# Kernel optimization log

Hardware: AMD Instinct MI355X
Metric: run time of the kernel (lower is better)

The kernel has to match this reference:

```python
import jax, jax.numpy as jnp
import numpy as np


def setup_inputs() -> dict:
    key = jax.random.key(0)
    k1, k2 = jax.random.split(key)
    N = 2_000_000
    rotation = jax.random.normal(k1, (N, 3, 3), dtype=jnp.float32)
    # learned parameter: eye(3) + 0.001 * randn(3,3)
    mat = jnp.eye(3, dtype=jnp.float32) + 0.001 * jax.random.normal(k2, (3, 3), dtype=jnp.float32)
    return {"rotation": rotation, "mat": mat}


def reference(rotation, mat):
    # new_mat[n] = rotation[n] @ mat   (mat broadcast over the batch)
    new_mat = jnp.einsum('nab,bc->nac', rotation, mat)
    # batched 3x3 SVD; polar orthogonal factor U @ V^T
    U, S, Vh = jnp.linalg.svd(new_mat, full_matrices=False)
    out = jnp.einsum('nab,nbc->nac', U, Vh)  # Vh is already V^T
    logdet = jnp.zeros((rotation.shape[0],), dtype=rotation.dtype)
    return out, logdet
```

## Files before the change

### kernel.cpp

```cpp
#include <hip/hip_runtime.h>
#include <math.h>

constexpr int BLOCK = 256;
constexpr int WPB = 4;

typedef __attribute__((address_space(3))) uint32_t lds_u32_t;
typedef __attribute__((address_space(1))) const uint32_t glb_u32_t;

__device__ __forceinline__ void issue_tile_loads(
    const float* __restrict__ rot, long long tile, int lane, float* buf)
{
    const char* g = (const char*)rot + (size_t)tile * 2304;
    __builtin_amdgcn_global_load_lds((glb_u32_t*)(g + (size_t)lane * 16),
                                     (lds_u32_t*)buf, 16, 0, 0);
    __builtin_amdgcn_global_load_lds((glb_u32_t*)(g + 1024 + (size_t)lane * 16),
                                     (lds_u32_t*)(buf + 256), 16, 0, 0);
    __builtin_amdgcn_global_load_lds((glb_u32_t*)(g + 2048 + (size_t)lane * 4),
                                     (lds_u32_t*)(buf + 512), 4, 0, 0);
}

__device__ __forceinline__ void polar_core_h(
    const float r0, const float r1, const float r2,
    const float r3, const float r4, const float r5,
    const float r6, const float r7, const float r8,
    const float m0, const float m1, const float m2,
    const float m3, const float m4, const float m5,
    const float m6, const float m7, const float m8,
    float& x0, float& x1, float& x2,
    float& x3, float& x4, float& x5,
    float& x6, float& x7, float& x8)
{
    const double dR = (double)r0*((double)r4*r8-(double)r5*r7)
                    - (double)r1*((double)r3*r8-(double)r5*r6)
                    + (double)r2*((double)r3*r7-(double)r4*r6);
    const float detA = (float)dR;

    x0=fmaf(r0,m0,fmaf(r1,m3,r2*m6));
    x1=fmaf(r0,m1,fmaf(r1,m4,r2*m7));
    x2=fmaf(r0,m2,fmaf(r1,m5,r2*m8));
    x3=fmaf(r3,m0,fmaf(r4,m3,r5*m6));
    x4=fmaf(r3,m1,fmaf(r4,m4,r5*m7));
    x5=fmaf(r3,m2,fmaf(r4,m5,r5*m8));
    x6=fmaf(r6,m0,fmaf(r7,m3,r8*m6));
    x7=fmaf(r6,m1,fmaf(r7,m4,r8*m7));
    x8=fmaf(r6,m2,fmaf(r7,m5,r8*m8));

    {
        const float c0=fmaf(x4,x8,-x5*x7), c1=fmaf(x5,x6,-x3*x8), c2=fmaf(x3,x7,-x4*x6);
        const float c3=fmaf(x2,x7,-x1*x8), c4=fmaf(x0,x8,-x2*x6), c5=fmaf(x1,x6,-x0*x7);
        const float c6=fmaf(x1,x5,-x2*x4), c7=fmaf(x2,x3,-x0*x5), c8=fmaf(x0,x4,-x1*x3);
        const float adet = fmaxf(fabsf(detA), 1e-30f);
        float nX2, nC2;
        { const float a=fmaf(x1,x1,x0*x0), b=fmaf(x3,x3,x2*x2),
                      e=fmaf(x5,x5,x4*x4), d=fmaf(x7,x7,x6*x6);
          nX2=(a+b)+(e+fmaf(x8,x8,d)); }
        { const float a=fmaf(c1,c1,c0*c0), b=fmaf(c3,c3,c2*c2),
                      e=fmaf(c5,c5,c4*c4), d=fmaf(c7,c7,c6*c6);
          nC2=(a+b)+(e+fmaf(c8,c8,d)); }
        const float h  = __builtin_amdgcn_rsqf(adet);
        const float pr = __builtin_amdgcn_sqrtf(__builtin_amdgcn_sqrtf(
                             nC2*__builtin_amdgcn_rcpf(nX2)));
        const float qr = __builtin_amdgcn_rcpf(pr);
        const float s = 0.5f*pr*h;
        const float t = copysignf(0.5f*qr*h, detA);
        x0=fmaf(s,x0,t*c0); x1=fmaf(s,x1,t*c1); x2=fmaf(s,x2,t*c2);
        x3=fmaf(s,x3,t*c3); x4=fmaf(s,x4,t*c4); x5=fmaf(s,x5,t*c5);
        x6=fmaf(s,x6,t*c6); x7=fmaf(s,x7,t*c7); x8=fmaf(s,x8,t*c8);
    }
    #pragma unroll
    for (int it = 0; it < 4; ++it) {
        const float c0=fmaf(x4,x8,-x5*x7), c1=fmaf(x5,x6,-x3*x8), c2=fmaf(x3,x7,-x4*x6);
        const float c3=fmaf(x2,x7,-x1*x8), c4=fmaf(x0,x8,-x2*x6), c5=fmaf(x1,x6,-x0*x7);
        const float c6=fmaf(x1,x5,-x2*x4), c7=fmaf(x2,x3,-x0*x5), c8=fmaf(x0,x4,-x1*x3);
        const float det = fmaf(x0,c0,fmaf(x1,c1,x2*c2));
        const float adet = fmaxf(fabsf(det), 1e-30f);
        const float mu = __builtin_amdgcn_exp2f(
                             -0.33333333f*__builtin_amdgcn_logf(adet));
        const float s = 0.5f*mu;
        const float t = copysignf(0.5f*__builtin_amdgcn_rcpf(mu*adet), det);
        x0=fmaf(s,x0,t*c0); x1=fmaf(s,x1,t*c1); x2=fmaf(s,x2,t*c2);
        x3=fmaf(s,x3,t*c3); x4=fmaf(s,x4,t*c4); x5=fmaf(s,x5,t*c5);
        x6=fmaf(s,x6,t*c6); x7=fmaf(s,x7,t*c7); x8=fmaf(s,x8,t*c8);
    }
    {
        const float c0=fmaf(x4,x8,-x5*x7), c1=fmaf(x5,x6,-x3*x8), c2=fmaf(x3,x7,-x4*x6);
        const float c3=fmaf(x2,x7,-x1*x8), c4=fmaf(x0,x8,-x2*x6), c5=fmaf(x1,x6,-x0*x7);
        const float c6=fmaf(x1,x5,-x2*x4), c7=fmaf(x2,x3,-x0*x5), c8=fmaf(x0,x4,-x1*x3);
        const float det = fmaf(x0,c0,fmaf(x1,c1,x2*c2));
        const float t = 0.5f*__builtin_amdgcn_rcpf(det);
        x0=fmaf(0.5f,x0,t*c0); x1=fmaf(0.5f,x1,t*c1); x2=fmaf(0.5f,x2,t*c2);
        x3=fmaf(0.5f,x3,t*c3); x4=fmaf(0.5f,x4,t*c4); x5=fmaf(0.5f,x5,t*c5);
        x6=fmaf(0.5f,x6,t*c6); x7=fmaf(0.5f,x7,t*c7); x8=fmaf(0.5f,x8,t*c8);
    }
}

__global__ __launch_bounds__(BLOCK) void polar3x3_kernel(
    const float* __restrict__ rot,
    const float* __restrict__ mat,
    float* __restrict__ outq,
    float* __restrict__ logdet,
    int N)
{
    __shared__ float lds[WPB * 2 * 576];
    const int lane = threadIdx.x & 63;
    const int wave = threadIdx.x >> 6;
    const long long W   = (long long)gridDim.x * WPB;
    const long long wid = (long long)blockIdx.x * WPB + wave;
    const int NT = N >> 6;

    const float m0=mat[0], m1=mat[1], m2=mat[2], m3=mat[3], m4=mat[4],
                m5=mat[5], m6=mat[6], m7=mat[7], m8=mat[8];
    asm volatile("s_waitcnt vmcnt(0) lgkmcnt(0)" ::: "memory");

    long long t = wid;
    if (t < NT) {
        float* bc = lds + wave * 1152;
        float* bn = bc + 576;
        issue_tile_loads(rot, t, lane, bc);
        { const long long t1 = t + W;
          issue_tile_loads(rot, (t1 < NT) ? t1 : 0, lane, bn); }
        asm volatile("s_waitcnt vmcnt(3)" ::: "memory");

        for (; t < NT; t += W) {
            const float* r = &bc[lane * 9];
            const float r0=r[0],r1=r[1],r2=r[2],r3=r[3],r4=r[4],
                        r5=r[5],r6=r[6],r7=r[7],r8=r[8];
            float x0,x1,x2,x3,x4,x5,x6,x7,x8;
            polar_core_h(r0,r1,r2,r3,r4,r5,r6,r7,r8,
                         m0,m1,m2,m3,m4,m5,m6,m7,m8,
                         x0,x1,x2,x3,x4,x5,x6,x7,x8);

            float* w = &bc[lane * 9];
            w[0]=x0; w[1]=x1; w[2]=x2; w[3]=x3; w[4]=x4;
            w[5]=x5; w[6]=x6; w[7]=x7; w[8]=x8;
            asm volatile("s_waitcnt lgkmcnt(0)" ::: "memory");

            const long long mb = t * 64;
            float* gdst = outq + mb * 9;
            const float4* l4 = (const float4*)bc;
            float4* g4 = (float4*)gdst;
            g4[lane]         = l4[lane];
            g4[64 + lane]    = l4[64 + lane];
            gdst[512 + lane] = bc[512 + lane];
            logdet[mb + lane] = 0.0f;

            asm volatile("" ::: "memory");

            { const long long tn = t + 2*W;
              issue_tile_loads(rot, (tn < NT) ? tn : 0, lane, bc); }

            asm volatile("s_waitcnt vmcnt(7)" ::: "memory");

            float* tmp = bc; bc = bn; bn = tmp;
        }
    }

    const int rem = N - NT * 64;
    if (rem > 0 && wid == 0) {
        const long long tb = (long long)NT * 64;
        const bool act = lane < rem;
        float r0=1.f,r1=0.f,r2=0.f,r3=0.f,r4=1.f,r5=0.f,r6=0.f,r7=0.f,r8=1.f;
        const float* gsrc = rot + (tb + lane) * 9;
        if (act) { r0=gsrc[0];r1=gsrc[1];r2=gsrc[2];r3=gsrc[3];r4=gsrc[4];
                   r5=gsrc[5];r6=gsrc[6];r7=gsrc[7];r8=gsrc[8]; }
        float x0,x1,x2,x3,x4,x5,x6,x7,x8;
        polar_core_h(r0,r1,r2,r3,r4,r5,r6,r7,r8,
                     m0,m1,m2,m3,m4,m5,m6,m7,m8,
                     x0,x1,x2,x3,x4,x5,x6,x7,x8);
        if (act) {
            float* gdst = outq + (tb + lane) * 9;
            gdst[0]=x0; gdst[1]=x1; gdst[2]=x2; gdst[3]=x3; gdst[4]=x4;
            gdst[5]=x5; gdst[6]=x6; gdst[7]=x7; gdst[8]=x8;
            logdet[tb + lane] = 0.0f;
        }
    }
}

extern "C" void kernel_launch(void* const* d_in, const int* in_sizes, int n_in,
                              void* d_out, int out_size, void* d_ws, size_t ws_size,
                              hipStream_t stream) {
    const float* rot = (const float*)d_in[0];
    const float* mat = (const float*)d_in[1];
    float* out = (float*)d_out;
    const int N = in_sizes[0] / 9;
    float* logdet = out + (long long)N * 9;
    const int NT = N >> 6;
    long long nb = ((long long)NT + WPB - 1) / WPB;
    if (nb > 2048) nb = 2048;
    if (nb < 1) nb = 1;
    polar3x3_kernel<<<(int)nb, BLOCK, 0, stream>>>(rot, mat, out, logdet, N);
}
```

Before: 139.4 us.

## Warp-specialize block into a loader wave and three compute waves

```diff
diff --git a/kernel.cpp b/kernel.cpp
--- a/kernel.cpp
+++ b/kernel.cpp
@@ -2,10 +2,16 @@
 #include <math.h>
 
 constexpr int BLOCK = 256;
-constexpr int WPB = 4;
+constexpr int NCONS = 3;
+constexpr int NSLOT = 3;
 
 typedef __attribute__((address_space(3))) uint32_t lds_u32_t;
 typedef __attribute__((address_space(1))) const uint32_t glb_u32_t;
+
+#define FENCE() asm volatile("" ::: "memory")
+__device__ __forceinline__ void BAR() {
+    FENCE(); __builtin_amdgcn_s_barrier(); FENCE();
+}
 
 __device__ __forceinline__ void issue_tile_loads(
     const float* __restrict__ rot, long long tile, int lane, float* buf)
@@ -101,62 +107,72 @@
     float* __restrict__ logdet,
     int N)
 {
-    __shared__ float lds[WPB * 2 * 576];
+    __shared__ float lds[NCONS * NSLOT * 576];
     const int lane = threadIdx.x & 63;
     const int wave = threadIdx.x >> 6;
-    const long long W   = (long long)gridDim.x * WPB;
-    const long long wid = (long long)blockIdx.x * WPB + wave;
     const int NT = N >> 6;
+    const long long CW = (long long)gridDim.x * NCONS;
+    const int nrounds = (int)(((long long)NT + CW - 1) / CW);
 
     const float m0=mat[0], m1=mat[1], m2=mat[2], m3=mat[3], m4=mat[4],
                 m5=mat[5], m6=mat[6], m7=mat[7], m8=mat[8];
     asm volatile("s_waitcnt vmcnt(0) lgkmcnt(0)" ::: "memory");
 
-    long long t = wid;
-    if (t < NT) {
-        float* bc = lds + wave * 1152;
-        float* bn = bc + 576;
-        issue_tile_loads(rot, t, lane, bc);
-        { const long long t1 = t + W;
-          issue_tile_loads(rot, (t1 < NT) ? t1 : 0, lane, bn); }
-        asm volatile("s_waitcnt vmcnt(3)" ::: "memory");
-
-        for (; t < NT; t += W) {
-            const float* r = &bc[lane * 9];
-            const float r0=r[0],r1=r[1],r2=r[2],r3=r[3],r4=r[4],
-                        r5=r[5],r6=r[6],r7=r[7],r8=r[8];
-            float x0,x1,x2,x3,x4,x5,x6,x7,x8;
-            polar_core_h(r0,r1,r2,r3,r4,r5,r6,r7,r8,
-                         m0,m1,m2,m3,m4,m5,m6,m7,m8,
-                         x0,x1,x2,x3,x4,x5,x6,x7,x8);
-
-            float* w = &bc[lane * 9];
-            w[0]=x0; w[1]=x1; w[2]=x2; w[3]=x3; w[4]=x4;
-            w[5]=x5; w[6]=x6; w[7]=x7; w[8]=x8;
-            asm volatile("s_waitcnt lgkmcnt(0)" ::: "memory");
-
-            const long long mb = t * 64;
-            float* gdst = outq + mb * 9;
-            const float4* l4 = (const float4*)bc;
-            float4* g4 = (float4*)gdst;
-            g4[lane]         = l4[lane];
-            g4[64 + lane]    = l4[64 + lane];
-            gdst[512 + lane] = bc[512 + lane];
-            logdet[mb + lane] = 0.0f;
-
-            asm volatile("" ::: "memory");
-
-            { const long long tn = t + 2*W;
-              issue_tile_loads(rot, (tn < NT) ? tn : 0, lane, bc); }
-
-            asm volatile("s_waitcnt vmcnt(7)" ::: "memory");
-
-            float* tmp = bc; bc = bn; bn = tmp;
+    if (wave == NCONS) {
+        for (int r = 0; r < 2; ++r) {
+            for (int c = 0; c < NCONS; ++c) {
+                long long t = (long long)r * CW + (long long)blockIdx.x * NCONS + c;
+                if (t >= NT) t = 0;
+                issue_tile_loads(rot, t, lane,
+                                 &lds[(c * NSLOT + (r % NSLOT)) * 576]);
+            }
+        }
+        asm volatile("s_waitcnt vmcnt(9)" ::: "memory");
+        BAR();
+        for (int r = 0; r < nrounds; ++r) {
+            for (int c = 0; c < NCONS; ++c) {
+                long long t = (long long)(r + 2) * CW + (long long)blockIdx.x * NCONS + c;
+                if (t >= NT) t = 0;
+                issue_tile_loads(rot, t, lane,
+                                 &lds[(c * NSLOT + ((r + 2) % NSLOT)) * 576]);
+            }
+            asm volatile("s_waitcnt vmcnt(9)" ::: "memory");
+            BAR();
+        }
+    } else {
+        const int c = wave;
+        float* ring = &lds[c * NSLOT * 576];
+        BAR();
+        for (int r = 0; r < nrounds; ++r) {
+            const long long t = (long long)r * CW + (long long)blockIdx.x * NCONS + c;
+            if (t < NT) {
+                float* buf = ring + (r % NSLOT) * 576;
+                const float* rd = &buf[lane * 9];
+                const float r0=rd[0],r1=rd[1],r2=rd[2],r3=rd[3],r4=rd[4],
+                            r5=rd[5],r6=rd[6],r7=rd[7],r8=rd[8];
+                float x0,x1,x2,x3,x4,x5,x6,x7,x8;
+                polar_core_h(r0,r1,r2,r3,r4,r5,r6,r7,r8,
+                             m0,m1,m2,m3,m4,m5,m6,m7,m8,
+                             x0,x1,x2,x3,x4,x5,x6,x7,x8);
+                float* w = &buf[lane * 9];
+                w[0]=x0; w[1]=x1; w[2]=x2; w[3]=x3; w[4]=x4;
+                w[5]=x5; w[6]=x6; w[7]=x7; w[8]=x8;
+                asm volatile("s_waitcnt lgkmcnt(0)" ::: "memory");
+                const long long mb = t * 64;
+                float* gdst = outq + mb * 9;
+                const float4* l4 = (const float4*)buf;
+                float4* g4 = (float4*)gdst;
+                g4[lane]         = l4[lane];
+                g4[64 + lane]    = l4[64 + lane];
+                gdst[512 + lane] = buf[512 + lane];
+                logdet[mb + lane] = 0.0f;
+            }
+            BAR();
         }
     }
 
     const int rem = N - NT * 64;
-    if (rem > 0 && wid == 0) {
+    if (rem > 0 && blockIdx.x == 0 && wave == 0) {
         const long long tb = (long long)NT * 64;
         const bool act = lane < rem;
         float r0=1.f,r1=0.f,r2=0.f,r3=0.f,r4=1.f,r5=0.f,r6=0.f,r7=0.f,r8=1.f;
@@ -185,8 +201,8 @@
     const int N = in_sizes[0] / 9;
     float* logdet = out + (long long)N * 9;
     const int NT = N >> 6;
-    long long nb = ((long long)NT + WPB - 1) / WPB;
-    if (nb > 2048) nb = 2048;
+    long long nb = ((long long)NT + NCONS - 1) / NCONS;
+    if (nb > 1792) nb = 1792;
     if (nb < 1) nb = 1;
     polar3x3_kernel<<<(int)nb, BLOCK, 0, stream>>>(rot, mat, out, logdet, N);
 }
```

Result: no change. 137.7 us (-1.3%).

## Replace persistent grid-stride loop with one-shot waves of two tiles and nontemporal stores

Applied to the files above, without the earlier changes.

```diff
diff --git a/kernel.cpp b/kernel.cpp
--- a/kernel.cpp
+++ b/kernel.cpp
@@ -94,6 +94,24 @@
     }
 }
 
+__device__ __forceinline__ void store_matrix_nt(
+    float* __restrict__ outq, float* __restrict__ logdet, long long m,
+    float x0, float x1, float x2, float x3, float x4,
+    float x5, float x6, float x7, float x8)
+{
+    float* g = outq + m * 9;
+    __builtin_nontemporal_store(x0, g + 0);
+    __builtin_nontemporal_store(x1, g + 1);
+    __builtin_nontemporal_store(x2, g + 2);
+    __builtin_nontemporal_store(x3, g + 3);
+    __builtin_nontemporal_store(x4, g + 4);
+    __builtin_nontemporal_store(x5, g + 5);
+    __builtin_nontemporal_store(x6, g + 6);
+    __builtin_nontemporal_store(x7, g + 7);
+    __builtin_nontemporal_store(x8, g + 8);
+    __builtin_nontemporal_store(0.0f, logdet + m);
+}
+
 __global__ __launch_bounds__(BLOCK) void polar3x3_kernel(
     const float* __restrict__ rot,
     const float* __restrict__ mat,
@@ -104,74 +122,63 @@
     __shared__ float lds[WPB * 2 * 576];
     const int lane = threadIdx.x & 63;
     const int wave = threadIdx.x >> 6;
-    const long long W   = (long long)gridDim.x * WPB;
-    const long long wid = (long long)blockIdx.x * WPB + wave;
-    const int NT = N >> 6;
+    const long long wid   = (long long)blockIdx.x * WPB + wave;
+    const long long base0 = wid * 128;
+    if (base0 >= N) return;
+
+    float* ldsA = lds + wave * 1152;
+    float* ldsB = ldsA + 576;
 
     const float m0=mat[0], m1=mat[1], m2=mat[2], m3=mat[3], m4=mat[4],
                 m5=mat[5], m6=mat[6], m7=mat[7], m8=mat[8];
     asm volatile("s_waitcnt vmcnt(0) lgkmcnt(0)" ::: "memory");
 
-    long long t = wid;
-    if (t < NT) {
-        float* bc = lds + wave * 1152;
-        float* bn = bc + 576;
-        issue_tile_loads(rot, t, lane, bc);
-        { const long long t1 = t + W;
-          issue_tile_loads(rot, (t1 < NT) ? t1 : 0, lane, bn); }
+    if (N - base0 >= 128) {
+        issue_tile_loads(rot, base0 >> 6, lane, ldsA);
+        issue_tile_loads(rot, (base0 >> 6) + 1, lane, ldsB);
         asm volatile("s_waitcnt vmcnt(3)" ::: "memory");
 
-        for (; t < NT; t += W) {
-            const float* r = &bc[lane * 9];
+        float xa0,xa1,xa2,xa3,xa4,xa5,xa6,xa7,xa8;
+        {
+            const float* r = &ldsA[lane * 9];
+            const float r0=r[0],r1=r[1],r2=r[2],r3=r[3],r4=r[4],
+                        r5=r[5],r6=r[6],r7=r[7],r8=r[8];
+            polar_core_h(r0,r1,r2,r3,r4,r5,r6,r7,r8,
+                         m0,m1,m2,m3,m4,m5,m6,m7,m8,
+                         xa0,xa1,xa2,xa3,xa4,xa5,xa6,xa7,xa8);
+        }
+
+        asm volatile("s_waitcnt vmcnt(0)" ::: "memory");
+
+        store_matrix_nt(outq, logdet, base0 + lane,
+                        xa0,xa1,xa2,xa3,xa4,xa5,xa6,xa7,xa8);
+
+        {
+            const float* r = &ldsB[lane * 9];
             const float r0=r[0],r1=r[1],r2=r[2],r3=r[3],r4=r[4],
                         r5=r[5],r6=r[6],r7=r[7],r8=r[8];
             float x0,x1,x2,x3,x4,x5,x6,x7,x8;
             polar_core_h(r0,r1,r2,r3,r4,r5,r6,r7,r8,
                          m0,m1,m2,m3,m4,m5,m6,m7,m8,
                          x0,x1,x2,x3,x4,x5,x6,x7,x8);
-
-            float* w = &bc[lane * 9];
-            w[0]=x0; w[1]=x1; w[2]=x2; w[3]=x3; w[4]=x4;
-            w[5]=x5; w[6]=x6; w[7]=x7; w[8]=x8;
-            asm volatile("s_waitcnt lgkmcnt(0)" ::: "memory");
-
-            const long long mb = t * 64;
-            float* gdst = outq + mb * 9;
-            const float4* l4 = (const float4*)bc;
-            float4* g4 = (float4*)gdst;
-            g4[lane]         = l4[lane];
-            g4[64 + lane]    = l4[64 + lane];
-            gdst[512 + lane] = bc[512 + lane];
-            logdet[mb + lane] = 0.0f;
-
-            asm volatile("" ::: "memory");
-
-            { const long long tn = t + 2*W;
-              issue_tile_loads(rot, (tn < NT) ? tn : 0, lane, bc); }
-
-            asm volatile("s_waitcnt vmcnt(7)" ::: "memory");
-
-            float* tmp = bc; bc = bn; bn = tmp;
+            store_matrix_nt(outq, logdet, base0 + 64 + lane,
+                            x0,x1,x2,x3,x4,x5,x6,x7,x8);
         }
-    }
-
-    const int rem = N - NT * 64;
-    if (rem > 0 && wid == 0) {
-        const long long tb = (long long)NT * 64;
-        const bool act = lane < rem;
-        float r0=1.f,r1=0.f,r2=0.f,r3=0.f,r4=1.f,r5=0.f,r6=0.f,r7=0.f,r8=1.f;
-        const float* gsrc = rot + (tb + lane) * 9;
-        if (act) { r0=gsrc[0];r1=gsrc[1];r2=gsrc[2];r3=gsrc[3];r4=gsrc[4];
-                   r5=gsrc[5];r6=gsrc[6];r7=gsrc[7];r8=gsrc[8]; }
-        float x0,x1,x2,x3,x4,x5,x6,x7,x8;
-        polar_core_h(r0,r1,r2,r3,r4,r5,r6,r7,r8,
-                     m0,m1,m2,m3,m4,m5,m6,m7,m8,
-                     x0,x1,x2,x3,x4,x5,x6,x7,x8);
-        if (act) {
-            float* gdst = outq + (tb + lane) * 9;
-            gdst[0]=x0; gdst[1]=x1; gdst[2]=x2; gdst[3]=x3; gdst[4]=x4;
-            gdst[5]=x5; gdst[6]=x6; gdst[7]=x7; gdst[8]=x8;
-            logdet[tb + lane] = 0.0f;
+    } else {
+        for (int t = 0; t < 2; ++t) {
+            const long long tb = base0 + (long long)t * 64;
+            if (tb >= N) break;
+            if (tb + lane < N) {
+                const float* gsrc = rot + (tb + lane) * 9;
+                const float r0=gsrc[0],r1=gsrc[1],r2=gsrc[2],r3=gsrc[3],
+                            r4=gsrc[4],r5=gsrc[5],r6=gsrc[6],r7=gsrc[7],r8=gsrc[8];
+                float x0,x1,x2,x3,x4,x5,x6,x7,x8;
+                polar_core_h(r0,r1,r2,r3,r4,r5,r6,r7,r8,
+                             m0,m1,m2,m3,m4,m5,m6,m7,m8,
+                             x0,x1,x2,x3,x4,x5,x6,x7,x8);
+                store_matrix_nt(outq, logdet, tb + lane,
+                                x0,x1,x2,x3,x4,x5,x6,x7,x8);
+            }
         }
     }
 }
@@ -184,9 +191,7 @@
     float* out = (float*)d_out;
     const int N = in_sizes[0] / 9;
     float* logdet = out + (long long)N * 9;
-    const int NT = N >> 6;
-    long long nb = ((long long)NT + WPB - 1) / WPB;
-    if (nb > 2048) nb = 2048;
-    if (nb < 1) nb = 1;
-    polar3x3_kernel<<<(int)nb, BLOCK, 0, stream>>>(rot, mat, out, logdet, N);
+    const long long nwaves  = ((long long)N + 127) / 128;
+    const int nblocks = (int)((nwaves + 3) / 4);
+    polar3x3_kernel<<<nblocks, BLOCK, 0, stream>>>(rot, mat, out, logdet, N);
 }
```

Result: slower. 160.7 us (+15.2%).
